# Kernel tuning notes

Measured on AMD Instinct MI355X. Metric: run time of the kernel, lower is better.

## Reference

```python
import jax, jax.numpy as jnp
import numpy as np

DIM, HEADS, EXPERTS, DFF = 1024, 16, 8, 4096
EPS = 1e-5

def layernorm(x, g, b):
    mu = jnp.mean(x, -1, keepdims=True)
    var = jnp.mean(jnp.square(x - mu), -1, keepdims=True)
    return (x - mu) * jax.lax.rsqrt(var + EPS) * g + b

def setup_inputs() -> dict:
    key = jax.random.key(0)
    ks = jax.random.split(key, 12)
    s = lambda d: 1.0 / np.sqrt(d)
    return {
        "x": jax.random.normal(ks[0], (2, 2048, DIM), jnp.float32),
        "conv_w": jax.random.normal(ks[1], (DIM, DIM, 3), jnp.float32) * s(DIM * 3),
        "conv_b": jnp.zeros((DIM,), jnp.float32),
        "wqkv": jax.random.normal(ks[2], (3 * DIM, DIM), jnp.float32) * s(DIM),
        "bqkv": jnp.zeros((3 * DIM,), jnp.float32),
        "wo": jax.random.normal(ks[3], (DIM, DIM), jnp.float32) * s(DIM),
        "bo": jnp.zeros((DIM,), jnp.float32),
        "ln1_g": jnp.ones((DIM,), jnp.float32),
        "ln1_b": jnp.zeros((DIM,), jnp.float32),
        "gate_w": jax.random.normal(ks[4], (DIM, EXPERTS), jnp.float32) * s(DIM),
        "gate_b": jnp.zeros((EXPERTS,), jnp.float32),
        "w1": jax.random.normal(ks[5], (EXPERTS, DIM, DFF), jnp.float32) * s(DIM),
        "b1": jnp.zeros((EXPERTS, DFF), jnp.float32),
        "w2": jax.random.normal(ks[6], (EXPERTS, DFF, DIM), jnp.float32) * s(DFF),
        "b2": jnp.zeros((EXPERTS, DIM), jnp.float32),
        "ln2_g": jnp.ones((DIM,), jnp.float32),
        "ln2_b": jnp.zeros((DIM,), jnp.float32),
    }

def reference(x, conv_w, conv_b, wqkv, bqkv, wo, bo, ln1_g, ln1_b,
              gate_w, gate_b, w1, b1, w2, b2, ln2_g, ln2_b):
    B, S, D = x.shape
    H, dh = HEADS, D // HEADS
    # Conv1d over sequence (channels = dim), padding=1
    xt = jnp.transpose(x, (0, 2, 1))  # (B, D, S)
    xt = jax.lax.conv_general_dilated(xt, conv_w, (1,), [(1, 1)],
                                      dimension_numbers=("NCH", "OIH", "NCH"))
    x = jnp.transpose(xt + conv_b[None, :, None], (0, 2, 1))  # (B, S, D)
    # Multi-head self-attention (batch_first semantics)
    qkv = x @ wqkv.T + bqkv  # (B, S, 3D)
    q, k, v = jnp.split(qkv, 3, axis=-1)
    q = q.reshape(B, S, H, dh).transpose(0, 2, 1, 3)
    k = k.reshape(B, S, H, dh).transpose(0, 2, 1, 3)
    v = v.reshape(B, S, H, dh).transpose(0, 2, 1, 3)
    scores = jnp.einsum("bhqd,bhkd->bhqk", q, k) / jnp.sqrt(jnp.float32(dh))
    attn = jax.nn.softmax(scores, axis=-1)
    ctx = jnp.einsum("bhqk,bhkd->bhqd", attn, v)
    ctx = ctx.transpose(0, 2, 1, 3).reshape(B, S, D)
    attn_out = ctx @ wo.T + bo
    x = layernorm(x + attn_out, ln1_g, ln1_b)
    # MoE: softmax gate over experts, dense weighted combine of expert FFNs
    probs = jax.nn.softmax(x @ gate_w + gate_b, axis=-1)  # (B, S, E)
    h = jax.nn.relu(jnp.einsum("bsd,edf->bsef", x, w1) + b1)  # (B, S, E, DFF)
    y = jnp.einsum("bsef,efd->bsed", h, w2) + b2  # (B, S, E, D)
    moe_out = jnp.einsum("bse,bsed->bsd", probs, y)
    x = layernorm(x + moe_out, ln2_g, ln2_b)
    return x
```

## Files before the change

kernel.cpp:

```cpp
#include <hip/hip_runtime.h>

#define SEQ   2048
#define NBAT  2
#define MTOT  4096
#define DIMC  1024
#define DFFC  4096
#define NEXP  8
#define NHEAD 16

typedef unsigned short u16;
typedef unsigned int   u32;
typedef unsigned long long u64;
typedef __attribute__((ext_vector_type(8)))  _Float16       f16x8;
typedef __attribute__((ext_vector_type(8)))  unsigned short us8;
typedef __attribute__((ext_vector_type(4)))  float          f32x4;
typedef __attribute__((ext_vector_type(16))) float          f32x16;

__device__ __forceinline__ u16 cvt16(float a) {
  return __builtin_bit_cast(u16, (_Float16)a);
}
__device__ __forceinline__ f16x8 ld_f16(const u16* p) {
  return __builtin_bit_cast(f16x8, *(const us8*)p);
}
__device__ __forceinline__ f32x4 mfma16(f16x8 a, f16x8 b, f32x4 c) {
  return __builtin_amdgcn_mfma_f32_16x16x32_f16(a, b, c, 0, 0, 0);
}
__device__ __forceinline__ f32x16 mfma32f(f16x8 a, f16x8 b, f32x16 c) {
  return __builtin_amdgcn_mfma_f32_32x32x16_f16(a, b, c, 0, 0, 0);
}
__device__ __forceinline__ void gload16(const u16* g, u16* l) {
  __builtin_amdgcn_global_load_lds(
      (const __attribute__((address_space(1))) void*)g,
      (__attribute__((address_space(3))) void*)l, 16, 0, 0);
}

template<bool WF32, bool WF16>
__global__ __launch_bounds__(256)
void pgemm16_kernel(const u16* __restrict__ A16, int lda,
                    const u16* __restrict__ B16, int ldb, int K,
                    float* __restrict__ Cf, u16* __restrict__ Ch, int ldc,
                    const float* __restrict__ bias,
                    const float* __restrict__ residual,
                    const float* __restrict__ row_scale, int rs_stride,
                    int do_relu, int do_accum,
                    int zmode, long sAZ, long sBZ, long sCZ, int sbias)
{
  const int z = blockIdx.z;
  if (zmode == 1) {
    B16 += (size_t)z * sBZ;
    Ch  += (size_t)z * sCZ;
    bias += (size_t)z * sbias;
  } else if (zmode == 2) {
    const int par = z >> 1, kh = z & 1;
    A16 += (size_t)par * sAZ + kh * 2048;
    B16 += (size_t)par * sBZ + kh * 2048;
    Cf  += (size_t)z * sCZ;
    bias = kh ? bias + (size_t)par * sbias : nullptr;
    row_scale += par;
  } else if (zmode == 3) {
    A16 += (size_t)z * sAZ;  B16 += (size_t)z * sAZ;
    Cf  += (size_t)z * sCZ;
    if (!z) { bias = nullptr; residual = nullptr; }
  }

  const int gx = gridDim.x;
  int bid = blockIdx.y * gx + blockIdx.x;
  const int cpx = (gx * gridDim.y) >> 3;
  bid = (bid & 7) * cpx + (bid >> 3);
  const int m0 = (bid / gx) * 128, n0 = (bid % gx) * 128;

  __shared__ __align__(16) u16 As[2][128][32];
  __shared__ __align__(16) u16 Bs[2][128][32];
  const int t = threadIdx.x;
  const int wid = t >> 6, lane = t & 63;
  const int wr = wid >> 1, wc = wid & 1;
  const int l15 = lane & 15, l4 = lane >> 4;

  f32x4 acc[4][4];
#pragma unroll
  for (int i = 0; i < 4; ++i)
#pragma unroll
    for (int j = 0; j < 4; ++j)
#pragma unroll
      for (int r = 0; r < 4; ++r) acc[i][j][r] = 0.f;

  const int rs0 = (wid * 2) * 16 + (lane >> 2);
  const int rs1 = (wid * 2 + 1) * 16 + (lane >> 2);
  const int cs  = (((lane & 3) ^ ((lane >> 3) & 3))) * 8;
  const int slot0 = (wid * 2) * 512, slot1 = (wid * 2 + 1) * 512;
  const u16* gA0 = A16 + (size_t)(m0 + rs0) * lda + cs;
  const u16* gA1 = A16 + (size_t)(m0 + rs1) * lda + cs;
  const u16* gB0 = B16 + (size_t)(n0 + rs0) * ldb + cs;
  const u16* gB1 = B16 + (size_t)(n0 + rs1) * ldb + cs;

#define STAGE(k0_, b_)                                        \
  {                                                           \
    gload16(gA0 + (k0_), (u16*)As[b_] + slot0);               \
    gload16(gA1 + (k0_), (u16*)As[b_] + slot1);               \
    gload16(gB0 + (k0_), (u16*)Bs[b_] + slot0);               \
    gload16(gB1 + (k0_), (u16*)Bs[b_] + slot1);               \
  }

  const int fswz = ((l15 >> 1) & 3);

#define COMPUTE(b_)                                                          \
  {                                                                          \
    f16x8 af[4], bf[4];                                                      \
    _Pragma("unroll")                                                        \
    for (int mf = 0; mf < 4; ++mf)                                           \
      af[mf] = ld_f16(&As[b_][wr * 64 + mf * 16 + l15][(l4 ^ fswz) * 8]);    \
    _Pragma("unroll")                                                        \
    for (int nf = 0; nf < 4; ++nf)                                           \
      bf[nf] = ld_f16(&Bs[b_][wc * 64 + nf * 16 + l15][(l4 ^ fswz) * 8]);    \
    __builtin_amdgcn_s_setprio(1);                                           \
    _Pragma("unroll")                                                        \
    for (int mf = 0; mf < 4; ++mf)                                           \
      _Pragma("unroll")                                                      \
      for (int nf = 0; nf < 4; ++nf)                                         \
        acc[mf][nf] = mfma16(af[mf], bf[nf], acc[mf][nf]);                   \
    __builtin_amdgcn_s_setprio(0);                                           \
  }

  const int NT = K >> 5;
  STAGE(0, 0);
  STAGE(32, 1);
  int cur = 0;
  for (int tt = 0; tt < NT - 2; ++tt) {
    asm volatile("s_waitcnt vmcnt(4)" ::: "memory");
    __builtin_amdgcn_s_barrier();
    COMPUTE(cur);
    __builtin_amdgcn_s_barrier();
    STAGE((tt + 2) << 5, cur);
    cur ^= 1;
  }
  asm volatile("s_waitcnt vmcnt(4)" ::: "memory");
  __builtin_amdgcn_s_barrier();
  COMPUTE(cur);
  asm volatile("s_waitcnt vmcnt(0)" ::: "memory");
  __builtin_amdgcn_s_barrier();
  COMPUTE(cur ^ 1);
#undef STAGE
#undef COMPUTE

#pragma unroll
  for (int mf = 0; mf < 4; ++mf)
#pragma unroll
    for (int nf = 0; nf < 4; ++nf) {
      const int col = n0 + wc * 64 + nf * 16 + l15;
      const float bia = bias ? bias[col] : 0.f;
#pragma unroll
      for (int r = 0; r < 4; ++r) {
        const int row = m0 + wr * 64 + mf * 16 + l4 * 4 + r;
        float v = acc[mf][nf][r] + bia;
        if (do_relu)   v = fmaxf(v, 0.f);
        if (row_scale) v *= row_scale[(size_t)row * rs_stride];
        if (residual)  v += residual[(size_t)row * ldc + col];
        if (WF32) {
          float* cp = &Cf[(size_t)row * ldc + col];
          float vv = v;
          if (do_accum) vv += *cp;
          *cp = vv;
        }
        if (WF16) Ch[(size_t)row * ldc + col] = cvt16(v);
      }
    }
}

__global__ __launch_bounds__(256)
void cvt_rows16_kernel(const float* __restrict__ in, u16* __restrict__ o, long n4)
{
  const long g = (long)blockIdx.x * 256 + threadIdx.x;
  if (g >= n4) return;
  const float4 v = *(const float4*)&in[g * 4];
  union { u16 s[4]; u64 v64; } p;
  p.s[0] = cvt16(v.x); p.s[1] = cvt16(v.y); p.s[2] = cvt16(v.z); p.s[3] = cvt16(v.w);
  *(u64*)&o[g * 4] = p.v64;
}

__global__ __launch_bounds__(256)
void cvt_T16_kernel(const float* __restrict__ in, u16* __restrict__ o, int R, int C)
{
  __shared__ float tile[32][33];
  const size_t zo = (size_t)blockIdx.z * R * C;
  in += zo; o += zo;
  const int tx = threadIdx.x, ty = threadIdx.y;
  const int r0 = blockIdx.y * 32, c0 = blockIdx.x * 32;
#pragma unroll
  for (int i = 0; i < 4; ++i)
    tile[ty + i * 8][tx] = in[(size_t)(r0 + ty + i * 8) * C + c0 + tx];
  __syncthreads();
#pragma unroll
  for (int i = 0; i < 4; ++i)
    o[(size_t)(c0 + ty + i * 8) * R + r0 + tx] = cvt16(tile[tx][ty + i * 8]);
}

__global__ __launch_bounds__(256)
void im2c16_kernel(const float* __restrict__ x, u16* __restrict__ o)
{
  const long g = (long)blockIdx.x * 256 + threadIdx.x;
  if (g >= (long)MTOT * 3072 / 4) return;
  const long id4 = g * 4;
  const int j = (int)(id4 % 3072);
  const int m = (int)(id4 / 3072);
  const int tt = j >> 10, i = j & 1023;
  const int b = m >> 11, s = m & 2047;
  const int sr = s + tt - 1;
  float4 v = make_float4(0.f, 0.f, 0.f, 0.f);
  if (sr >= 0 && sr < SEQ) v = *(const float4*)&x[((size_t)(b * SEQ + sr) << 10) + i];
  union { u16 s[4]; u64 v64; } p;
  p.s[0] = cvt16(v.x); p.s[1] = cvt16(v.y); p.s[2] = cvt16(v.z); p.s[3] = cvt16(v.w);
  *(u64*)&o[id4] = p.v64;
}

__global__ __launch_bounds__(256)
void wpk16_kernel(const float* __restrict__ cw, u16* __restrict__ o)
{
  const long g = (long)blockIdx.x * 256 + threadIdx.x;
  if (g >= (long)1024 * 3072 / 4) return;
  const long id4 = g * 4;
  const int oc = (int)(id4 / 3072);
  const int kp = (int)(id4 % 3072);
  const int tt = kp >> 10, i = kp & 1023;
  union { u16 s[4]; u64 v64; } p;
#pragma unroll
  for (int q = 0; q < 4; ++q)
    p.s[q] = cvt16(cw[(size_t)oc * 3072 + (i + q) * 3 + tt]);
  *(u64*)&o[id4] = p.v64;
}

__global__ __launch_bounds__(256)
void attn16_kernel(const u16* __restrict__ qkv, u16* __restrict__ ctx16)
{
  const int qt = blockIdx.x, h = blockIdx.y, b = blockIdx.z;
  const int t = threadIdx.x;
  const int w = t >> 6, lane = t & 63;
  const int l31 = lane & 31, half = lane >> 5;

  __shared__ __align__(16) u16 Ks[64 * 64];
  __shared__ __align__(16) u16 Vt[64 * 64];

  const size_t base = (size_t)b * SEQ * 3072;
  const int hoff = h * 64;
  const int q0 = qt * 128 + w * 32;

  f16x8 qh[4];
  {
    const u16* qrow = &qkv[base + (size_t)(q0 + l31) * 3072 + hoff];
#pragma unroll
    for (int ks = 0; ks < 4; ++ks) qh[ks] = ld_f16(&qrow[ks * 16 + half * 8]);
  }

  f32x16 cf[2];
#pragma unroll
  for (int nf = 0; nf < 2; ++nf)
#pragma unroll
    for (int r = 0; r < 16; ++r) cf[nf][r] = 0.f;
  float m_run = -1e30f, l_run = 0.f;

  const int kkey = t >> 2, kc = t & 3;
  const int vd = t & 63, vkg = t >> 6;

  for (int kt = 0; kt < SEQ / 64; ++kt) {
    __syncthreads();
    {
      const u16* kr = &qkv[base + (size_t)(kt * 64 + kkey) * 3072 + 1024 + hoff];
      const int swz = (kkey & 7) << 4;
#pragma unroll
      for (int i = 0; i < 2; ++i) {
        const us8 v = *(const us8*)&kr[kc * 16 + i * 8];
        *(us8*)((char*)Ks + kkey * 128 + ((kc * 32 + i * 16) ^ swz)) = v;
      }
    }
    {
      const u16* vc = &qkv[base + (size_t)(kt * 64 + vkg * 16) * 3072 + 2048 + hoff + vd];
      union { u16 s[8]; us8 v8; } V0, V1;
#pragma unroll
      for (int i = 0; i < 8; ++i) {
        V0.s[i] = vc[(size_t)i * 3072];
        V1.s[i] = vc[(size_t)(i + 8) * 3072];
      }
      const int swz = (vd & 7) << 4;
      *(us8*)((char*)Vt + vd * 128 + ((vkg * 32) ^ swz))      = V0.v8;
      *(us8*)((char*)Vt + vd * 128 + ((vkg * 32 + 16) ^ swz)) = V1.v8;
    }
    __syncthreads();

    f32x16 sf[2];
#pragma unroll
    for (int f = 0; f < 2; ++f)
#pragma unroll
      for (int r = 0; r < 16; ++r) sf[f][r] = 0.f;
#pragma unroll
    for (int ks = 0; ks < 4; ++ks) {
      const int rb = ks * 32 + half * 16;
#pragma unroll
      for (int f = 0; f < 2; ++f) {
        const int key = f * 32 + l31;
        const int off = rb ^ ((key & 7) << 4);
        const f16x8 kh = __builtin_bit_cast(f16x8, *(const us8*)((char*)Ks + key * 128 + off));
        sf[f] = mfma32f(kh, qh[ks], sf[f]);
      }
    }

    float tmax = -1e30f;
#pragma unroll
    for (int f = 0; f < 2; ++f)
#pragma unroll
      for (int r = 0; r < 16; ++r) tmax = fmaxf(tmax, sf[f][r]);
    tmax *= 0.125f;
    tmax = fmaxf(tmax, __shfl_xor(tmax, 32, 64));
    const float m_new = fmaxf(m_run, tmax);
    const float resc = __expf(m_run - m_new);
    float lt = 0.f;
#pragma unroll
    for (int f = 0; f < 2; ++f)
#pragma unroll
      for (int r = 0; r < 16; ++r) {
        const float p = __expf(__builtin_fmaf(sf[f][r], 0.125f, -m_new));
        sf[f][r] = p; lt += p;
      }
    lt += __shfl_xor(lt, 32, 64);
    l_run = l_run * resc + lt;
    m_run = m_new;
#pragma unroll
    for (int r = 0; r < 16; ++r) {
      const int qr = (r & 3) + 8 * (r >> 2) + 4 * half;
      const float rs = __shfl(resc, qr, 64);
      cf[0][r] *= rs; cf[1][r] *= rs;
    }

    u32 W0[2][4], W1[2][4];
#pragma unroll
    for (int f = 0; f < 2; ++f)
#pragma unroll
      for (int g = 0; g < 4; ++g) {
        auto p0 = __builtin_amdgcn_cvt_pkrtz(sf[f][4 * g], sf[f][4 * g + 1]);
        auto p1 = __builtin_amdgcn_cvt_pkrtz(sf[f][4 * g + 2], sf[f][4 * g + 3]);
        W0[f][g] = __builtin_bit_cast(u32, p0);
        W1[f][g] = __builtin_bit_cast(u32, p1);
      }
    f16x8 PA[4];
#pragma unroll
    for (int ks = 0; ks < 4; ++ks) {
      const int f = ks >> 1, g0 = (ks & 1) * 2;
      u32 a = W0[f][g0], b2 = W0[f][g0 + 1];
      u32 c = W1[f][g0], d2 = W1[f][g0 + 1];
      asm volatile("v_permlane32_swap_b32 %0, %1" : "+v"(a), "+v"(b2));
      asm volatile("v_permlane32_swap_b32 %0, %1" : "+v"(c), "+v"(d2));
      union { u32 w[4]; us8 v8; } pa;
      pa.w[0] = a; pa.w[1] = c; pa.w[2] = b2; pa.w[3] = d2;
      PA[ks] = __builtin_bit_cast(f16x8, pa.v8);
    }

#pragma unroll
    for (int ks = 0; ks < 4; ++ks) {
      const int rb = ks * 32 + half * 16;
#pragma unroll
      for (int nf = 0; nf < 2; ++nf) {
        const int dd = nf * 32 + l31;
        const int off = rb ^ ((dd & 7) << 4);
        const f16x8 vh = __builtin_bit_cast(f16x8, *(const us8*)((char*)Vt + dd * 128 + off));
        cf[nf] = mfma32f(PA[ks], vh, cf[nf]);
      }
    }
  }

  const float invl = 1.f / l_run;
#pragma unroll
  for (int r = 0; r < 16; ++r) {
    const int qr = (r & 3) + 8 * (r >> 2) + 4 * half;
    const float il = __shfl(invl, qr, 64);
    const size_t row = (size_t)(b * SEQ + q0 + qr) * 1024 + hoff;
#pragma unroll
    for (int nf = 0; nf < 2; ++nf)
      ctx16[row + nf * 32 + l31] = cvt16(cf[nf][r] * il);
  }
}

__global__ __launch_bounds__(256)
void ln_kernel(const float* __restrict__ in, const float* __restrict__ res,
               int nres, long rstride,
               const float* __restrict__ g, const float* __restrict__ bt,
               float* __restrict__ outf, u16* __restrict__ outh)
{
  const int row = blockIdx.x, t = threadIdx.x;
  const size_t off = ((size_t)row << 10) + t * 4;
  float4 v = *(const float4*)&in[off];
  for (int i = 0; i < nres; ++i) {
    const float4 r = *(const float4*)&res[off + (size_t)i * rstride];
    v.x += r.x; v.y += r.y; v.z += r.z; v.w += r.w;
  }
  float s  = v.x + v.y + v.z + v.w;
  float ss = v.x * v.x + v.y * v.y + v.z * v.z + v.w * v.w;
#pragma unroll
  for (int o = 32; o; o >>= 1) {
    s  += __shfl_xor(s, o, 64);
    ss += __shfl_xor(ss, o, 64);
  }
  __shared__ float red[8];
  if ((t & 63) == 0) { red[(t >> 6) * 2] = s; red[(t >> 6) * 2 + 1] = ss; }
  __syncthreads();
  s  = red[0] + red[2] + red[4] + red[6];
  ss = red[1] + red[3] + red[5] + red[7];
  const float mu   = s * (1.f / 1024.f);
  const float var  = ss * (1.f / 1024.f) - mu * mu;
  const float rstd = rsqrtf(var + 1e-5f);
  const float4 gg = *(const float4*)&g[t * 4];
  const float4 bb = *(const float4*)&bt[t * 4];
  float4 o;
  o.x = (v.x - mu) * rstd * gg.x + bb.x;
  o.y = (v.y - mu) * rstd * gg.y + bb.y;
  o.z = (v.z - mu) * rstd * gg.z + bb.z;
  o.w = (v.w - mu) * rstd * gg.w + bb.w;
  if (outf) *(float4*)&outf[off] = o;
  if (outh) {
    union { u16 s[4]; u64 v64; } p;
    p.s[0] = cvt16(o.x); p.s[1] = cvt16(o.y); p.s[2] = cvt16(o.z); p.s[3] = cvt16(o.w);
    *(u64*)&outh[off] = p.v64;
  }
}

__global__ __launch_bounds__(64)
void gate_kernel(const float* __restrict__ x, const float* __restrict__ gw,
                 const float* __restrict__ gb, float* __restrict__ probs)
{
  const int m = blockIdx.x, lane = threadIdx.x;
  float acc[8];
#pragma unroll
  for (int e = 0; e < 8; ++e) acc[e] = 0.f;
  for (int k = lane; k < 1024; k += 64) {
    const float xv = x[((size_t)m << 10) + k];
    const float4 g0 = *(const float4*)&gw[k * 8];
    const float4 g1 = *(const float4*)&gw[k * 8 + 4];
    acc[0] = __builtin_fmaf(xv, g0.x, acc[0]);
    acc[1] = __builtin_fmaf(xv, g0.y, acc[1]);
    acc[2] = __builtin_fmaf(xv, g0.z, acc[2]);
    acc[3] = __builtin_fmaf(xv, g0.w, acc[3]);
    acc[4] = __builtin_fmaf(xv, g1.x, acc[4]);
    acc[5] = __builtin_fmaf(xv, g1.y, acc[5]);
    acc[6] = __builtin_fmaf(xv, g1.z, acc[6]);
    acc[7] = __builtin_fmaf(xv, g1.w, acc[7]);
  }
#pragma unroll
  for (int o = 32; o; o >>= 1)
#pragma unroll
    for (int e = 0; e < 8; ++e) acc[e] += __shfl_xor(acc[e], o, 64);
  float lg[8], mx = -1e30f;
#pragma unroll
  for (int e = 0; e < 8; ++e) { lg[e] = acc[e] + gb[e]; mx = fmaxf(mx, lg[e]); }
  float se = 0.f;
#pragma unroll
  for (int e = 0; e < 8; ++e) { lg[e] = __expf(lg[e] - mx); se += lg[e]; }
  const float inv = 1.f / se;
  if (lane < 8) probs[(size_t)m * 8 + lane] = lg[lane] * inv;
}

extern "C" void kernel_launch(void* const* d_in, const int* in_sizes, int n_in,
                              void* d_out, int out_size, void* d_ws, size_t ws_size,
                              hipStream_t stream)
{
  const float* x      = (const float*)d_in[0];
  const float* conv_w = (const float*)d_in[1];
  const float* conv_b = (const float*)d_in[2];
  const float* wqkv   = (const float*)d_in[3];
  const float* bqkv   = (const float*)d_in[4];
  const float* wo     = (const float*)d_in[5];
  const float* bo     = (const float*)d_in[6];
  const float* ln1_g  = (const float*)d_in[7];
  const float* ln1_b  = (const float*)d_in[8];
  const float* gate_w = (const float*)d_in[9];
  const float* gate_b = (const float*)d_in[10];
  const float* w1     = (const float*)d_in[11];
  const float* b1     = (const float*)d_in[12];
  const float* w2     = (const float*)d_in[13];
  const float* b2     = (const float*)d_in[14];
  const float* ln2_g  = (const float*)d_in[15];
  const float* ln2_b  = (const float*)d_in[16];
  float* out = (float*)d_out;

  const dim3 blk256(256);
  char* W = (char*)d_ws;
#define MB(x) ((size_t)(x) << 20)
  float* x1_f   = (float*)(W + MB(0));
  float* moe_f  = (float*)(W + MB(16));
  float* probs  = (float*)(W + MB(144));
  u16* x1_h     = (u16*)(W + MB(145));
  u16* ctx16    = (u16*)(W + MB(153));
  u16* h16      = (u16*)(W + MB(161));
  u16* im2c16   = (u16*)(W + MB(161));
  u16* wpk16    = (u16*)(W + MB(185));
  u16* wqkv16   = (u16*)(W + MB(191));
  float* yconv_f= (float*)(W + MB(197));
  u16* yconv16  = (u16*)(W + MB(213));
  u16* qkv16    = (u16*)(W + MB(221));
  u16* wo16     = (u16*)(W + MB(245));
  float* res1a  = (float*)(W + MB(247));
  float* res1b  = (float*)(W + MB(263));
  u16* w1s16    = (u16*)(W + MB(289));
  u16* w2s16    = (u16*)(W + MB(353));

  im2c16_kernel<<<dim3(12288), blk256, 0, stream>>>(x, im2c16);
  wpk16_kernel<<<dim3(3072), blk256, 0, stream>>>(conv_w, wpk16);
  cvt_rows16_kernel<<<dim3(3072), blk256, 0, stream>>>(wqkv, wqkv16, 786432);
  cvt_rows16_kernel<<<dim3(1024), blk256, 0, stream>>>(wo, wo16, 262144);
  cvt_T16_kernel<<<dim3(128, 32, 8), dim3(32, 8), 0, stream>>>(w1, w1s16, 1024, 4096);
  cvt_T16_kernel<<<dim3(32, 128, 8), dim3(32, 8), 0, stream>>>(w2, w2s16, 4096, 1024);

  pgemm16_kernel<true, true><<<dim3(8, 32, 1), blk256, 0, stream>>>(
      im2c16, 3072, wpk16, 3072, 3072,
      yconv_f, yconv16, 1024,
      conv_b, nullptr, nullptr, 0, 0, 0, 0, 0, 0, 0, 0);

  pgemm16_kernel<false, true><<<dim3(24, 32, 1), blk256, 0, stream>>>(
      yconv16, 1024, wqkv16, 1024, 1024,
      nullptr, qkv16, 3072,
      bqkv, nullptr, nullptr, 0, 0, 0, 0, 0, 0, 0, 0);

  attn16_kernel<<<dim3(SEQ / 128, NHEAD, NBAT), blk256, 0, stream>>>(qkv16, ctx16);

  pgemm16_kernel<true, false><<<dim3(8, 32, 2), blk256, 0, stream>>>(
      ctx16, 1024, wo16, 1024, 512,
      res1a, nullptr, 1024,
      bo, yconv_f, nullptr, 0, 0, 0,
      3, 512, 0, 4194304, 0);

  ln_kernel<<<dim3(MTOT), blk256, 0, stream>>>(
      res1a, res1b, 1, 0, ln1_g, ln1_b, x1_f, x1_h);

  gate_kernel<<<dim3(MTOT), dim3(64), 0, stream>>>(x1_f, gate_w, gate_b, probs);

  pgemm16_kernel<false, true><<<dim3(32, 32, 4), blk256, 0, stream>>>(
      x1_h, 1024, w1s16, 1024, 1024,
      nullptr, h16, 4096,
      b1, nullptr, nullptr, 0, 1 , 0,
      1, 0, 4194304, 16777216, 4096);
  pgemm16_kernel<true, false><<<dim3(8, 32, 8), blk256, 0, stream>>>(
      h16, 4096, w2s16, 4096, 2048 ,
      moe_f, nullptr, 1024,
      b2, nullptr, probs, 8, 0, 0 ,
      2, 16777216, 4194304, 4194304, 1024);

  pgemm16_kernel<false, true><<<dim3(32, 32, 4), blk256, 0, stream>>>(
      x1_h, 1024, w1s16 + (size_t)4 * 4194304, 1024, 1024,
      nullptr, h16, 4096,
      b1 + 4 * 4096, nullptr, nullptr, 0, 1, 0,
      1, 0, 4194304, 16777216, 4096);
  pgemm16_kernel<true, false><<<dim3(8, 32, 8), blk256, 0, stream>>>(
      h16, 4096, w2s16 + (size_t)4 * 4194304, 4096, 2048,
      moe_f, nullptr, 1024,
      b2 + 4 * 1024, nullptr, probs + 4, 8, 0, 1 ,
      2, 16777216, 4194304, 4194304, 1024);

  ln_kernel<<<dim3(MTOT), blk256, 0, stream>>>(
      x1_f, moe_f, 8, 4194304, ln2_g, ln2_b, out, nullptr);
#undef MB
}
```

Measured before the change: 1.423 ms.

## Triple-buffer GEMM LDS staging and flatten grid with XCD-aware swizzle across z

The fp16 MFMA GEMM now uses three LDS stages instead of two, prefetching two tiles ahead so global loads have more time to complete before they are consumed. The grid is flattened to 1D and the block remap that spreads blocks over the eight XCDs now includes the z (expert/split) dimension, which changes which tiles share an L2. LDS per block rises from 32KB to 48KB, which could lower occupancy. The K loop drain and buffer rotation are adjusted to match.

```diff
diff --git a/kernel.cpp b/kernel.cpp
--- a/kernel.cpp
+++ b/kernel.cpp
@@ -43,9 +43,19 @@
                     const float* __restrict__ residual,
                     const float* __restrict__ row_scale, int rs_stride,
                     int do_relu, int do_accum,
+                    int nx, int ny,
                     int zmode, long sAZ, long sBZ, long sCZ, int sbias)
 {
-  const int z = blockIdx.z;
+  const int bid = blockIdx.x;
+  const int cpx = gridDim.x >> 3;
+  const int g   = (bid & 7) * cpx + (bid >> 3);
+  const int slice = nx * ny;
+  const int z  = g / slice;
+  const int r  = g - z * slice;
+  const int bx = r / ny;
+  const int by = r - bx * ny;
+  const int m0 = by * 128, n0 = bx * 128;
+
   if (zmode == 1) {
     B16 += (size_t)z * sBZ;
     Ch  += (size_t)z * sCZ;
@@ -63,14 +73,8 @@
     if (!z) { bias = nullptr; residual = nullptr; }
   }
 
-  const int gx = gridDim.x;
-  int bid = blockIdx.y * gx + blockIdx.x;
-  const int cpx = (gx * gridDim.y) >> 3;
-  bid = (bid & 7) * cpx + (bid >> 3);
-  const int m0 = (bid / gx) * 128, n0 = (bid % gx) * 128;
-
-  __shared__ __align__(16) u16 As[2][128][32];
-  __shared__ __align__(16) u16 Bs[2][128][32];
+  __shared__ __align__(16) u16 As[3][128][32];
+  __shared__ __align__(16) u16 Bs[3][128][32];
   const int t = threadIdx.x;
   const int wid = t >> 6, lane = t & 63;
   const int wr = wid >> 1, wc = wid & 1;
@@ -82,7 +86,7 @@
 #pragma unroll
     for (int j = 0; j < 4; ++j)
 #pragma unroll
-      for (int r = 0; r < 4; ++r) acc[i][j][r] = 0.f;
+      for (int r2 = 0; r2 < 4; ++r2) acc[i][j][r2] = 0.f;
 
   const int rs0 = (wid * 2) * 16 + (lane >> 2);
   const int rs1 = (wid * 2 + 1) * 16 + (lane >> 2);
@@ -124,21 +128,27 @@
   const int NT = K >> 5;
   STAGE(0, 0);
   STAGE(32, 1);
+  STAGE(64, 2);
   int cur = 0;
-  for (int tt = 0; tt < NT - 2; ++tt) {
-    asm volatile("s_waitcnt vmcnt(4)" ::: "memory");
+  for (int tt = 0; tt < NT - 3; ++tt) {
+    asm volatile("s_waitcnt vmcnt(8)" ::: "memory");
     __builtin_amdgcn_s_barrier();
     COMPUTE(cur);
     __builtin_amdgcn_s_barrier();
-    STAGE((tt + 2) << 5, cur);
-    cur ^= 1;
-  }
+    STAGE((tt + 3) << 5, cur);
+    cur = (cur == 2) ? 0 : cur + 1;
+  }
+  asm volatile("s_waitcnt vmcnt(8)" ::: "memory");
+  __builtin_amdgcn_s_barrier();
+  COMPUTE(cur);
+  cur = (cur == 2) ? 0 : cur + 1;
   asm volatile("s_waitcnt vmcnt(4)" ::: "memory");
   __builtin_amdgcn_s_barrier();
   COMPUTE(cur);
+  cur = (cur == 2) ? 0 : cur + 1;
   asm volatile("s_waitcnt vmcnt(0)" ::: "memory");
   __builtin_amdgcn_s_barrier();
-  COMPUTE(cur ^ 1);
+  COMPUTE(cur);
 #undef STAGE
 #undef COMPUTE
 
@@ -149,9 +159,9 @@
       const int col = n0 + wc * 64 + nf * 16 + l15;
       const float bia = bias ? bias[col] : 0.f;
 #pragma unroll
-      for (int r = 0; r < 4; ++r) {
-        const int row = m0 + wr * 64 + mf * 16 + l4 * 4 + r;
-        float v = acc[mf][nf][r] + bia;
+      for (int r2 = 0; r2 < 4; ++r2) {
+        const int row = m0 + wr * 64 + mf * 16 + l4 * 4 + r2;
+        float v = acc[mf][nf][r2] + bia;
         if (do_relu)   v = fmaxf(v, 0.f);
         if (row_scale) v *= row_scale[(size_t)row * rs_stride];
         if (residual)  v += residual[(size_t)row * ldc + col];
@@ -506,50 +516,52 @@
   cvt_T16_kernel<<<dim3(128, 32, 8), dim3(32, 8), 0, stream>>>(w1, w1s16, 1024, 4096);
   cvt_T16_kernel<<<dim3(32, 128, 8), dim3(32, 8), 0, stream>>>(w2, w2s16, 4096, 1024);
 
-  pgemm16_kernel<true, true><<<dim3(8, 32, 1), blk256, 0, stream>>>(
+  pgemm16_kernel<true, true><<<dim3(8 * 32), blk256, 0, stream>>>(
       im2c16, 3072, wpk16, 3072, 3072,
       yconv_f, yconv16, 1024,
-      conv_b, nullptr, nullptr, 0, 0, 0, 0, 0, 0, 0, 0);
-
-  pgemm16_kernel<false, true><<<dim3(24, 32, 1), blk256, 0, stream>>>(
+      conv_b, nullptr, nullptr, 0, 0, 0,
+      8, 32, 0, 0, 0, 0, 0);
+
+  pgemm16_kernel<false, true><<<dim3(24 * 32), blk256, 0, stream>>>(
       yconv16, 1024, wqkv16, 1024, 1024,
       nullptr, qkv16, 3072,
-      bqkv, nullptr, nullptr, 0, 0, 0, 0, 0, 0, 0, 0);
+      bqkv, nullptr, nullptr, 0, 0, 0,
+      24, 32, 0, 0, 0, 0, 0);
 
   attn16_kernel<<<dim3(SEQ / 128, NHEAD, NBAT), blk256, 0, stream>>>(qkv16, ctx16);
 
-  pgemm16_kernel<true, false><<<dim3(8, 32, 2), blk256, 0, stream>>>(
+  pgemm16_kernel<true, false><<<dim3(8 * 32 * 2), blk256, 0, stream>>>(
       ctx16, 1024, wo16, 1024, 512,
       res1a, nullptr, 1024,
       bo, yconv_f, nullptr, 0, 0, 0,
-      3, 512, 0, 4194304, 0);
+      8, 32, 3, 512, 0, 4194304, 0);
 
   ln_kernel<<<dim3(MTOT), blk256, 0, stream>>>(
       res1a, res1b, 1, 0, ln1_g, ln1_b, x1_f, x1_h);
 
   gate_kernel<<<dim3(MTOT), dim3(64), 0, stream>>>(x1_f, gate_w, gate_b, probs);
 
-  pgemm16_kernel<false, true><<<dim3(32, 32, 4), blk256, 0, stream>>>(
+  pgemm16_kernel<false, true><<<dim3(32 * 32 * 4), blk256, 0, stream>>>(
       x1_h, 1024, w1s16, 1024, 1024,
       nullptr, h16, 4096,
       b1, nullptr, nullptr, 0, 1 , 0,
-      1, 0, 4194304, 16777216, 4096);
-  pgemm16_kernel<true, false><<<dim3(8, 32, 8), blk256, 0, stream>>>(
+      32, 32, 1, 0, 4194304, 16777216, 4096);
+  pgemm16_kernel<true, false><<<dim3(8 * 32 * 8), blk256, 0, stream>>>(
       h16, 4096, w2s16, 4096, 2048 ,
       moe_f, nullptr, 1024,
       b2, nullptr, probs, 8, 0, 0 ,
-      2, 16777216, 4194304, 4194304, 1024);
-
-  pgemm16_kernel<false, true><<<dim3(32, 32, 4), blk256, 0, stream>>>(
+      8, 32, 2, 16777216, 4194304, 4194304, 1024);
+
+  pgemm16_kernel<false, true><<<dim3(32 * 32 * 4), blk256, 0, stream>>>(
       x1_h, 1024, w1s16 + (size_t)4 * 4194304, 1024, 1024,
       nullptr, h16, 4096,
       b1 + 4 * 4096, nullptr, nullptr, 0, 1, 0,
-      1, 0, 4194304, 16777216, 4096);
-  pgemm16_kernel<true, false><<<dim3(8, 32, 8), blk256, 0, stream>>>(
+      32, 32, 1, 0, 4194304, 16777216, 4096);
+  pgemm16_kernel<true, false><<<dim3(8 * 32 * 8), blk256, 0, stream>>>(
       h16, 4096, w2s16 + (size_t)4 * 4194304, 4096, 2048,
       moe_f, nullptr, 1024,
       b2 + 4 * 1024, nullptr, probs + 4, 8, 0, 1 ,
-      2, 16777216, 4194304, 4194304, 1024);
+      8, 32, 2, 16777216, 4194304, 4194304, 1024);
 
   ln_kernel<<<dim3(MTOT), blk256, 0, stream>>>(
       x1_f, moe_f, 8, 4194304, ln2_g, ln2_b, out, nullptr);
```

Result: slower. 1.533 ms (+7.7%).

## Add 256x256-tile 4-stage pipelined GEMM kernel for MoE expert FFNs

Applied to the files above, without the earlier changes.

Adds a new GEMM kernel with 256x256 output tiles, 512 threads (8 waves), and a 4-deep LDS ring buffer filled by direct global-to-LDS loads. Stage loads for tile t+3 are interleaved between two halves of the MFMA work, and MFMA sections run at raised wave priority. The four MoE expert GEMM launches now use this kernel, meant to raise arithmetic intensity and hide memory latency on the dominant FFN GEMMs. The larger tiles cost more registers and 128KB of LDS per block, which lowers occupancy and cuts the number of blocks per launch.

```diff
diff --git a/kernel.cpp b/kernel.cpp
--- a/kernel.cpp
+++ b/kernel.cpp
@@ -35,15 +35,14 @@
 }
 
 template<bool WF32, bool WF16>
-__global__ __launch_bounds__(256)
-void pgemm16_kernel(const u16* __restrict__ A16, int lda,
-                    const u16* __restrict__ B16, int ldb, int K,
-                    float* __restrict__ Cf, u16* __restrict__ Ch, int ldc,
-                    const float* __restrict__ bias,
-                    const float* __restrict__ residual,
-                    const float* __restrict__ row_scale, int rs_stride,
-                    int do_relu, int do_accum,
-                    int zmode, long sAZ, long sBZ, long sCZ, int sbias)
+__global__ __launch_bounds__(512)
+void pgemm256_kernel(const u16* __restrict__ A16, int lda,
+                     const u16* __restrict__ B16, int ldb, int K,
+                     float* __restrict__ Cf, u16* __restrict__ Ch, int ldc,
+                     const float* __restrict__ bias,
+                     const float* __restrict__ row_scale, int rs_stride,
+                     int do_relu, int do_accum,
+                     int zmode, long sAZ, long sBZ, long sCZ, int sbias)
 {
   const int z = blockIdx.z;
   if (zmode == 1) {
@@ -57,7 +56,129 @@
     Cf  += (size_t)z * sCZ;
     bias = kh ? bias + (size_t)par * sbias : nullptr;
     row_scale += par;
-  } else if (zmode == 3) {
+  }
+
+  const int gx = gridDim.x;
+  int bid = blockIdx.y * gx + blockIdx.x;
+  const int cpx = (gx * gridDim.y) >> 3;
+  bid = (bid & 7) * cpx + (bid >> 3);
+  const int m0 = (bid / gx) * 256, n0 = (bid % gx) * 256;
+
+  __shared__ __align__(16) u16 As[4][256][32];
+  __shared__ __align__(16) u16 Bs[4][256][32];
+  const int t = threadIdx.x;
+  const int wid = t >> 6, lane = t & 63;
+  const int wr = wid >> 2, wc = wid & 3;
+  const int l15 = lane & 15, l4 = lane >> 4;
+  const int fswz = (l15 >> 1) & 3;
+
+  f32x4 acc[8][4];
+#pragma unroll
+  for (int i = 0; i < 8; ++i)
+#pragma unroll
+    for (int j = 0; j < 4; ++j)
+#pragma unroll
+      for (int r = 0; r < 4; ++r) acc[i][j][r] = 0.f;
+
+  const int srow = wid * 32 + (lane >> 2);
+  const int scol = ((lane & 3) ^ ((lane >> 3) & 3)) * 8;
+  const u16* gA = A16 + (size_t)(m0 + srow) * lda + scol;
+  const u16* gB = B16 + (size_t)(n0 + srow) * ldb + scol;
+  const int slot = wid * 32 * 32 + (lane >> 2) * 32;
+
+#define STG_A(k0_, s_, j_) gload16(gA + (size_t)(j_) * 16 * lda + (k0_), \
+                                   (u16*)As[s_] + slot + (j_) * 16 * 32)
+#define STG_B(k0_, s_, j_) gload16(gB + (size_t)(j_) * 16 * ldb + (k0_), \
+                                   (u16*)Bs[s_] + slot + (j_) * 16 * 32)
+#define STAGE_TILE(k0_, s_) { STG_A(k0_, s_, 0); STG_A(k0_, s_, 1); \
+                              STG_B(k0_, s_, 0); STG_B(k0_, s_, 1); }
+
+  const int NT = K >> 5;
+  STAGE_TILE(0, 0); STAGE_TILE(32, 1); STAGE_TILE(64, 2);
+
+  for (int tt = 0; tt < NT; ++tt) {
+    const int s = tt & 3;
+    if (tt < NT - 2)      asm volatile("s_waitcnt vmcnt(8)" ::: "memory");
+    else if (tt == NT-2)  asm volatile("s_waitcnt vmcnt(4)" ::: "memory");
+    else                  asm volatile("s_waitcnt vmcnt(0)" ::: "memory");
+    __builtin_amdgcn_s_barrier();
+
+    const bool dostage = (tt < NT - 3);
+    const int ks = (tt + 3) << 5, ss = (tt + 3) & 3;
+
+    if (dostage) { STG_A(ks, ss, 0); STG_A(ks, ss, 1); }
+    f16x8 bf[4];
+#pragma unroll
+    for (int nf = 0; nf < 4; ++nf)
+      bf[nf] = ld_f16(&Bs[s][wc * 64 + nf * 16 + l15][(l4 ^ fswz) * 8]);
+    {
+      f16x8 af[4];
+#pragma unroll
+      for (int mf = 0; mf < 4; ++mf)
+        af[mf] = ld_f16(&As[s][wr * 128 + mf * 16 + l15][(l4 ^ fswz) * 8]);
+      __builtin_amdgcn_s_setprio(1);
+#pragma unroll
+      for (int mf = 0; mf < 4; ++mf)
+#pragma unroll
+        for (int nf = 0; nf < 4; ++nf)
+          acc[mf][nf] = mfma16(af[mf], bf[nf], acc[mf][nf]);
+      __builtin_amdgcn_s_setprio(0);
+    }
+    if (dostage) { STG_B(ks, ss, 0); STG_B(ks, ss, 1); }
+    {
+      f16x8 af[4];
+#pragma unroll
+      for (int mf = 0; mf < 4; ++mf)
+        af[mf] = ld_f16(&As[s][wr * 128 + 64 + mf * 16 + l15][(l4 ^ fswz) * 8]);
+      __builtin_amdgcn_s_setprio(1);
+#pragma unroll
+      for (int mf = 0; mf < 4; ++mf)
+#pragma unroll
+        for (int nf = 0; nf < 4; ++nf)
+          acc[mf + 4][nf] = mfma16(af[mf], bf[nf], acc[mf + 4][nf]);
+      __builtin_amdgcn_s_setprio(0);
+    }
+  }
+#undef STG_A
+#undef STG_B
+#undef STAGE_TILE
+
+#pragma unroll
+  for (int mf = 0; mf < 8; ++mf)
+#pragma unroll
+    for (int nf = 0; nf < 4; ++nf) {
+      const int col = n0 + wc * 64 + nf * 16 + l15;
+      const float bia = bias ? bias[col] : 0.f;
+#pragma unroll
+      for (int r = 0; r < 4; ++r) {
+        const int row = m0 + wr * 128 + mf * 16 + l4 * 4 + r;
+        float v = acc[mf][nf][r] + bia;
+        if (do_relu)   v = fmaxf(v, 0.f);
+        if (row_scale) v *= row_scale[(size_t)row * rs_stride];
+        if (WF32) {
+          float* cp = &Cf[(size_t)row * ldc + col];
+          float vv = v;
+          if (do_accum) vv += *cp;
+          *cp = vv;
+        }
+        if (WF16) Ch[(size_t)row * ldc + col] = cvt16(v);
+      }
+    }
+}
+
+template<bool WF32, bool WF16>
+__global__ __launch_bounds__(256)
+void pgemm16_kernel(const u16* __restrict__ A16, int lda,
+                    const u16* __restrict__ B16, int ldb, int K,
+                    float* __restrict__ Cf, u16* __restrict__ Ch, int ldc,
+                    const float* __restrict__ bias,
+                    const float* __restrict__ residual,
+                    const float* __restrict__ row_scale, int rs_stride,
+                    int do_relu, int do_accum,
+                    int zmode, long sAZ, long sBZ, long sCZ, int sbias)
+{
+  const int z = blockIdx.z;
+  if (zmode == 3) {
     A16 += (size_t)z * sAZ;  B16 += (size_t)z * sAZ;
     Cf  += (size_t)z * sCZ;
     if (!z) { bias = nullptr; residual = nullptr; }
@@ -82,7 +203,7 @@
 #pragma unroll
     for (int j = 0; j < 4; ++j)
 #pragma unroll
-      for (int r = 0; r < 4; ++r) acc[i][j][r] = 0.f;
+      for (int r2 = 0; r2 < 4; ++r2) acc[i][j][r2] = 0.f;
 
   const int rs0 = (wid * 2) * 16 + (lane >> 2);
   const int rs1 = (wid * 2 + 1) * 16 + (lane >> 2);
@@ -149,9 +270,9 @@
       const int col = n0 + wc * 64 + nf * 16 + l15;
       const float bia = bias ? bias[col] : 0.f;
 #pragma unroll
-      for (int r = 0; r < 4; ++r) {
-        const int row = m0 + wr * 64 + mf * 16 + l4 * 4 + r;
-        float v = acc[mf][nf][r] + bia;
+      for (int r2 = 0; r2 < 4; ++r2) {
+        const int row = m0 + wr * 64 + mf * 16 + l4 * 4 + r2;
+        float v = acc[mf][nf][r2] + bia;
         if (do_relu)   v = fmaxf(v, 0.f);
         if (row_scale) v *= row_scale[(size_t)row * rs_stride];
         if (residual)  v += residual[(size_t)row * ldc + col];
@@ -529,26 +650,26 @@
 
   gate_kernel<<<dim3(MTOT), dim3(64), 0, stream>>>(x1_f, gate_w, gate_b, probs);
 
-  pgemm16_kernel<false, true><<<dim3(32, 32, 4), blk256, 0, stream>>>(
+  pgemm256_kernel<false, true><<<dim3(16, 16, 4), dim3(512), 0, stream>>>(
       x1_h, 1024, w1s16, 1024, 1024,
       nullptr, h16, 4096,
-      b1, nullptr, nullptr, 0, 1 , 0,
+      b1, nullptr, 0, 1 , 0,
       1, 0, 4194304, 16777216, 4096);
-  pgemm16_kernel<true, false><<<dim3(8, 32, 8), blk256, 0, stream>>>(
+  pgemm256_kernel<true, false><<<dim3(4, 16, 8), dim3(512), 0, stream>>>(
       h16, 4096, w2s16, 4096, 2048 ,
       moe_f, nullptr, 1024,
-      b2, nullptr, probs, 8, 0, 0 ,
+      b2, probs, 8, 0, 0 ,
       2, 16777216, 4194304, 4194304, 1024);
 
-  pgemm16_kernel<false, true><<<dim3(32, 32, 4), blk256, 0, stream>>>(
+  pgemm256_kernel<false, true><<<dim3(16, 16, 4), dim3(512), 0, stream>>>(
       x1_h, 1024, w1s16 + (size_t)4 * 4194304, 1024, 1024,
       nullptr, h16, 4096,
-      b1 + 4 * 4096, nullptr, nullptr, 0, 1, 0,
+      b1 + 4 * 4096, nullptr, 0, 1, 0,
       1, 0, 4194304, 16777216, 4096);
-  pgemm16_kernel<true, false><<<dim3(8, 32, 8), blk256, 0, stream>>>(
+  pgemm256_kernel<true, false><<<dim3(4, 16, 8), dim3(512), 0, stream>>>(
       h16, 4096, w2s16 + (size_t)4 * 4194304, 4096, 2048,
       moe_f, nullptr, 1024,
-      b2 + 4 * 1024, nullptr, probs + 4, 8, 0, 1 ,
+      b2 + 4 * 1024, probs + 4, 8, 0, 1 ,
       2, 16777216, 4194304, 4194304, 1024);
 
   ln_kernel<<<dim3(MTOT), blk256, 0, stream>>>(
```

New measurement: 1.394 ms. 1.02x faster.
